# Kernel optimization log

Hardware: AMD Instinct MI355X
Metric: run time of the kernel (lower is better)

The kernel has to match this reference:

```python
import jax, jax.numpy as jnp
import numpy as np
from functools import partial

HEADS = 16
EPS = 1e-12  # torch F.normalize eps


def _l2_normalize(z):
    n = jnp.linalg.norm(z, axis=-1, keepdims=True)
    return z / jnp.maximum(n, EPS)


def setup_inputs() -> dict:
    key = jax.random.key(0)
    kx, kq, kk, kv, ko, kf = jax.random.split(key, 6)
    B, S, D, L = 2, 2048, 1024, 1024
    scale = 0.02
    return {
        "x": jax.random.normal(kx, (B, S, D), dtype=jnp.float32),
        "Wq": jax.random.normal(kq, (D, L), dtype=jnp.float32) * scale,
        "Wk": jax.random.normal(kk, (D, L), dtype=jnp.float32) * scale,
        "Wv": jax.random.normal(kv, (D, L), dtype=jnp.float32) * scale,
        "Wo": jax.random.normal(ko, (L, D), dtype=jnp.float32) * scale,
        "Wff": jax.random.normal(kf, (D, D), dtype=jnp.float32) * scale,
    }


def reference(x, Wq, Wk, Wv, Wo, Wff):
    B, S, D = x.shape
    H = HEADS
    L = Wq.shape[1]
    dh = L // H

    def split_heads(t):  # [B,S,L] -> [B*H, S, dh]  ('b y (h x) -> (b h) y x')
        return t.reshape(B, S, H, dh).transpose(0, 2, 1, 3).reshape(B * H, S, dh)

    q = split_heads(x @ Wq)
    k = split_heads(x @ Wk)
    v = split_heads(x @ Wv)

    # scores[b, k, q] = <q_q, k_k> / sqrt(input_size)  (note: scale uses D, not dh)
    scores = jnp.einsum('bqd,bkd->bkq', q, k) / jnp.sqrt(jnp.asarray(D, x.dtype))
    # faithful quirk: softmax over the LAST axis, which here is the query axis
    attn = jax.nn.softmax(scores, axis=-1)  # [B*H, K, Q]
    # out[b, q, d] = sum_k attn[b, k, q] * v[b, k, d]
    out = jnp.einsum('bkq,bkv->bqv', attn, v)  # [B*H, S, dh]

    # '(b h) y x -> b y (h x)'
    z = out.reshape(B, H, S, dh).transpose(0, 2, 1, 3).reshape(B, S, L)
    z = z @ Wo  # output projection (dropout is identity in eval)

    z = _l2_normalize(z)          # F.normalize after attention
    z = z @ Wff                   # FFNN linear (bias=False, dropout=identity)
    z = _l2_normalize(z)          # FFNN normalize (n_dim=-1)
    z = jax.nn.gelu(z, approximate=False)  # torch nn.GELU default = exact erf
    return z
```

## Files before the change

### kernel.cpp

```cpp
#include <hip/hip_runtime.h>
#include <hip/hip_bf16.h>
#include <stdint.h>


typedef __attribute__((ext_vector_type(8))) short short8;
typedef __attribute__((ext_vector_type(4))) float floatx4;

#define MFMA_BF16(a, b, c) __builtin_amdgcn_mfma_f32_16x16x32_bf16((a), (b), (c), 0, 0, 0)

__device__ __forceinline__ float bf2f(unsigned short u) {
  union { unsigned int i; float f; } v; v.i = ((unsigned int)u) << 16; return v.f;
}
__device__ __forceinline__ unsigned short f2bf(float f) {
  __hip_bfloat16 h = __float2bfloat16(f);
  return *reinterpret_cast<unsigned short*>(&h);
}
__device__ __forceinline__ void gld_lds16(const void* g, void* l) {
  __builtin_amdgcn_global_load_lds((__attribute__((address_space(1))) void*)g,
                                   (__attribute__((address_space(3))) void*)l,
                                   16, 0, 0);
}

__global__ __launch_bounds__(256) void detect_dtype(const unsigned int* __restrict__ x,
                                                    int* __restrict__ flag)
{
  __shared__ int red[4];
  int ok = 0;
  for (int i = 0; i < 16; ++i) {
    const unsigned int w = x[threadIdx.x * 16 + i];
    const unsigned int e = (w >> 7) & 0xFF;
    ok += (e == 0 || (e >= 96 && e <= 144)) ? 1 : 0;
  }
  for (int off = 32; off > 0; off >>= 1) ok += __shfl_down(ok, off, 64);
  if ((threadIdx.x & 63) == 0) red[threadIdx.x >> 6] = ok;
  __syncthreads();
  if (threadIdx.x == 0)
    *flag = ((red[0] + red[1] + red[2] + red[3]) > 2048) ? 1 : 0;
}

__global__ __launch_bounds__(256) void cvt_x(const void* __restrict__ src,
                                             unsigned short* __restrict__ dst,
                                             const int* __restrict__ flag)
{
  const int i = blockIdx.x * 256 + threadIdx.x;
  if (*flag) {
    ((uint4*)dst)[i] = ((const uint4*)src)[i];
  } else {
    const float4 a = ((const float4*)src)[2 * i];
    const float4 b = ((const float4*)src)[2 * i + 1];
    unsigned short o[8] = {f2bf(a.x), f2bf(a.y), f2bf(a.z), f2bf(a.w),
                           f2bf(b.x), f2bf(b.y), f2bf(b.z), f2bf(b.w)};
    ((uint4*)dst)[i] = *(uint4*)o;
  }
}

__global__ __launch_bounds__(256) void gemm_bt_128x64(
    const unsigned short* __restrict__ A, const unsigned short* __restrict__ Bt,
    unsigned short* __restrict__ C, int M, int N, int K, int lda, int ldb, int ldc)
{
  __shared__ __align__(16) unsigned short sA[128 * 32];
  __shared__ __align__(16) unsigned short sB[64 * 32];
  const int tid = threadIdx.x;
  const int wave = tid >> 6, lane = tid & 63, l15 = lane & 15, quad = lane >> 4;
  const int m0 = blockIdx.x * 128, n0 = blockIdx.y * 64;

  const floatx4 z4 = {0.f, 0.f, 0.f, 0.f};
  floatx4 acc[2][4];
  for (int i = 0; i < 2; ++i) for (int j = 0; j < 4; ++j) acc[i][j] = z4;

  const int NK = K >> 5;
  auto stage = [&](int kt) {
    const int k0 = kt << 5;
    for (int j = 0; j < 2; ++j) {
      const int ci = j * 256 + wave * 64 + lane;
      gld_lds16(A + (size_t)(m0 + (ci >> 2)) * lda + k0 + (ci & 3) * 8,
                &sA[(j * 256 + wave * 64) * 8]);
    }
    {
      const int ci = wave * 64 + lane;
      gld_lds16(Bt + (size_t)(n0 + (ci >> 2)) * ldb + k0 + (ci & 3) * 8,
                &sB[(wave * 64) * 8]);
    }
  };

  stage(0);
  for (int kt = 0; kt < NK; ++kt) {
    __syncthreads();
    short8 af[2], bf[4];
    for (int mt = 0; mt < 2; ++mt)
      af[mt] = *(const short8*)&sA[(wave * 32 + mt * 16 + l15) * 32 + quad * 8];
    for (int nt = 0; nt < 4; ++nt)
      bf[nt] = *(const short8*)&sB[(nt * 16 + l15) * 32 + quad * 8];
    for (int mt = 0; mt < 2; ++mt)
      for (int nt = 0; nt < 4; ++nt)
        acc[mt][nt] = MFMA_BF16(af[mt], bf[nt], acc[mt][nt]);
    __syncthreads();
    if (kt + 1 < NK) stage(kt + 1);
  }
  for (int mt = 0; mt < 2; ++mt)
    for (int nt = 0; nt < 4; ++nt)
      for (int r = 0; r < 4; ++r) {
        const int row = m0 + wave * 32 + mt * 16 + quad * 4 + r;
        const int col = n0 + nt * 16 + l15;
        C[(size_t)row * ldc + col] = f2bf(acc[mt][nt][r]);
      }
}

__global__ __launch_bounds__(256) void w_transpose(const void* __restrict__ W,
                                                   unsigned short* __restrict__ WT,
                                                   const int* __restrict__ flag)
{
  __shared__ __align__(16) unsigned short tile[64 * 72];
  const int rb = blockIdx.x * 64, cb = blockIdx.y * 64;
  const int tid = threadIdx.x;
  const int r = tid >> 2, c = tid & 3;
  unsigned short tmp[16];
  if (*flag) {
    const unsigned short* src = (const unsigned short*)W + (size_t)(rb + r) * 1024 + cb + c * 16;
    *(uint4*)&tmp[0] = *(const uint4*)src;
    *(uint4*)&tmp[8] = *(const uint4*)(src + 8);
  } else {
    const float* src = (const float*)W + (size_t)(rb + r) * 1024 + cb + c * 16;
    for (int j = 0; j < 16; j += 4) {
      const float4 f = *(const float4*)(src + j);
      tmp[j + 0] = f2bf(f.x); tmp[j + 1] = f2bf(f.y);
      tmp[j + 2] = f2bf(f.z); tmp[j + 3] = f2bf(f.w);
    }
  }
  *(uint4*)&tile[r * 72 + c * 16] = *(uint4*)&tmp[0];
  *(uint4*)&tile[r * 72 + c * 16 + 8] = *(uint4*)&tmp[8];
  __syncthreads();
  const int oc = tid >> 2;
  unsigned short out[16];
  for (int j = 0; j < 16; ++j) out[j] = tile[(c * 16 + j) * 72 + oc];
  unsigned short* dst = WT + (size_t)(cb + oc) * 1024 + rb + c * 16;
  *(uint4*)dst = *(uint4*)&out[0];
  *(uint4*)(dst + 8) = *(uint4*)&out[8];
}

__global__ __launch_bounds__(256) void v_transpose(const unsigned short* __restrict__ QKV,
                                                   unsigned short* __restrict__ Vt)
{
  __shared__ __align__(16) unsigned short tile[64 * 72];
  const int bh = blockIdx.x, st = blockIdx.y;
  const int b = bh >> 4, h = bh & 15;
  const int tid = threadIdx.x;
  const int r = tid >> 2, c = tid & 3;
  const unsigned short* src =
      QKV + (size_t)(b * 2048 + st * 64 + r) * 3072 + 2048 + h * 64 + c * 16;
  *(uint4*)&tile[r * 72 + c * 16] = *(const uint4*)src;
  *(uint4*)&tile[r * 72 + c * 16 + 8] = *(const uint4*)(src + 8);
  __syncthreads();
  const int d = tid >> 2;
  unsigned short out[16];
  for (int j = 0; j < 16; ++j) out[j] = tile[(c * 16 + j) * 72 + d];
  unsigned short* dst = Vt + (size_t)bh * 64 * 2048 + (size_t)d * 2048 + st * 64 + c * 16;
  *(uint4*)dst = *(uint4*)&out[0];
  *(uint4*)(dst + 8) = *(uint4*)&out[8];
}

__global__ __launch_bounds__(256) void attn_stats(const unsigned short* __restrict__ QKV,
                                                  float* __restrict__ spart)
{
  __shared__ __align__(16) unsigned short sQ[2][8 * 512];
  const int bh = blockIdx.x, kb = blockIdx.y, qs = blockIdx.z;
  const int b = bh >> 4, h = bh & 15;
  const int tid = threadIdx.x;
  const int wave = tid >> 6, lane = tid & 63, l15 = lane & 15, quad = lane >> 4;
  const int kbase = kb * 128 + wave * 32;
  const size_t row0 = (size_t)b * 2048;
  const int qoff = h * 64, koff = 1024 + h * 64;
  const int qbase = qs * 512;

  short8 kf[2][2];
  for (int rt = 0; rt < 2; ++rt)
    for (int ks = 0; ks < 2; ++ks)
      kf[rt][ks] = *(const short8*)&QKV[(row0 + kbase + rt * 16 + l15) * 3072 +
                                        koff + ks * 32 + quad * 8];

  float l[2][4];
  for (int rt = 0; rt < 2; ++rt)
    for (int r = 0; r < 4; ++r) l[rt][r] = 0.f;

  auto stageQ = [&](int t) {
    const int qt0 = qbase + t * 64;
    for (int j = 0; j < 2; ++j) {
      const int f = wave * 2 + j;
      const int nt = f >> 1, ks = f & 1;
      gld_lds16(QKV + (row0 + qt0 + nt * 16 + l15) * 3072 + qoff + ks * 32 + quad * 8,
                &sQ[t & 1][f * 512]);
    }
  };

  const floatx4 z4 = {0.f, 0.f, 0.f, 0.f};
  stageQ(0);
  for (int t = 0; t < 8; ++t) {
    __syncthreads();
    if (t + 1 < 8) stageQ(t + 1);
    const unsigned short* sQt = sQ[t & 1];
    for (int nt = 0; nt < 4; ++nt) {
      const short8 bq0 = *(const short8*)&sQt[(nt * 2 + 0) * 512 + lane * 8];
      const short8 bq1 = *(const short8*)&sQt[(nt * 2 + 1) * 512 + lane * 8];
      for (int rt = 0; rt < 2; ++rt) {
        floatx4 acc = z4;
        acc = MFMA_BF16(kf[rt][0], bq0, acc);
        acc = MFMA_BF16(kf[rt][1], bq1, acc);
        for (int r = 0; r < 4; ++r)
          l[rt][r] += __expf(acc[r] * 0.03125f);
      }
    }
  }
  for (int rt = 0; rt < 2; ++rt)
    for (int r = 0; r < 4; ++r) {
      float ll = l[rt][r];
      ll += __shfl_xor(ll, 1, 64);
      ll += __shfl_xor(ll, 2, 64);
      ll += __shfl_xor(ll, 4, 64);
      ll += __shfl_xor(ll, 8, 64);
      if (l15 == 0) {
        const int krow = kbase + rt * 16 + quad * 4 + r;
        spart[(size_t)qs * 65536 + bh * 2048 + krow] = ll;
      }
    }
}

__global__ __launch_bounds__(256) void stats_combine(const float* __restrict__ spart,
                                                     float* __restrict__ rsum)
{
  const int i = blockIdx.x * 256 + threadIdx.x;
  rsum[i] = 1.0f / (spart[i] + spart[i + 65536] + spart[i + 131072] + spart[i + 196608]);
}

__global__ __launch_bounds__(256) void attn_pv(const unsigned short* __restrict__ QKV,
                                               const unsigned short* __restrict__ Vt,
                                               const float* __restrict__ rsum,
                                               unsigned short* __restrict__ Z1)
{
  __shared__ __align__(16) unsigned short sK[64 * 64];
  __shared__ __align__(16) unsigned short sV[64 * 64];
  __shared__ __align__(16) unsigned short sP[64 * 72];
  const int bh = blockIdx.x, qb = blockIdx.y;
  const int b = bh >> 4, h = bh & 15;
  const int tid = threadIdx.x;
  const int wave = tid >> 6, lane = tid & 63, l15 = lane & 15, quad = lane >> 4;
  const size_t row0 = (size_t)b * 2048;
  const int qoff = h * 64, koff = 1024 + h * 64;
  const int q0 = qb * 64;
  const int srow = lane >> 3, schk = (lane & 7) ^ ((lane >> 3) & 7);

  short8 qf[2];
  for (int ks = 0; ks < 2; ++ks)
    qf[ks] = *(const short8*)&QKV[(row0 + q0 + wave * 16 + l15) * 3072 +
                                  qoff + ks * 32 + quad * 8];

  const floatx4 z4 = {0.f, 0.f, 0.f, 0.f};
  floatx4 acco[4];
  for (int j = 0; j < 4; ++j) acco[j] = z4;

  const unsigned short* VtB = Vt + (size_t)bh * 64 * 2048;
  const float* rsB = rsum + bh * 2048;

  for (int kt = 0; kt < 32; ++kt) {
    const int kb = kt * 64;
    __syncthreads();
    for (int j = 0; j < 2; ++j) {
      const int jj = wave * 2 + j;
      gld_lds16(QKV + (row0 + kb + jj * 8 + srow) * 3072 + koff + schk * 8, &sK[jj * 512]);
      gld_lds16(VtB + (size_t)(jj * 8 + srow) * 2048 + kb + schk * 8, &sV[jj * 512]);
    }
    __syncthreads();
    floatx4 sacc[4];
    for (int nt = 0; nt < 4; ++nt) {
      floatx4 a = z4;
      for (int ks = 0; ks < 2; ++ks) {
        const int row = nt * 16 + l15;
        const int chk = (ks * 4 + quad) ^ (l15 & 7);
        const short8 kfr = *(const short8*)&sK[row * 64 + chk * 8];
        a = MFMA_BF16(qf[ks], kfr, a);
      }
      sacc[nt] = a;
    }
    for (int nt = 0; nt < 4; ++nt) {
      const float rc = rsB[kb + nt * 16 + l15];
      for (int r = 0; r < 4; ++r) {
        const float p = __expf(sacc[nt][r] * 0.03125f) * rc;
        sP[(wave * 16 + quad * 4 + r) * 72 + nt * 16 + l15] = f2bf(p);
      }
    }
    __syncthreads();
    for (int ks = 0; ks < 2; ++ks) {
      const short8 pf = *(const short8*)&sP[(wave * 16 + l15) * 72 + ks * 32 + quad * 8];
      for (int nt = 0; nt < 4; ++nt) {
        const int row = nt * 16 + l15;
        const int chk = (ks * 4 + quad) ^ (l15 & 7);
        const short8 vf = *(const short8*)&sV[row * 64 + chk * 8];
        acco[nt] = MFMA_BF16(pf, vf, acco[nt]);
      }
    }
  }
  for (int nt = 0; nt < 4; ++nt)
    for (int r = 0; r < 4; ++r) {
      const int q = q0 + wave * 16 + quad * 4 + r;
      const int d = nt * 16 + l15;
      Z1[(row0 + q) * 1024 + qoff + d] = f2bf(acco[nt][r]);
    }
}

__global__ __launch_bounds__(256) void l2norm_gelu(const unsigned short* __restrict__ in,
                                                   void* __restrict__ out, int do_gelu,
                                                   int fin, const int* __restrict__ flag)
{
  __shared__ float red[4];
  const int row = blockIdx.x, tid = threadIdx.x;
  const unsigned short* p = in + (size_t)row * 1024 + tid * 4;
  const ushort4 u = *(const ushort4*)p;
  float x[4] = {bf2f(u.x), bf2f(u.y), bf2f(u.z), bf2f(u.w)};
  float ss = x[0] * x[0] + x[1] * x[1] + x[2] * x[2] + x[3] * x[3];
  for (int off = 32; off > 0; off >>= 1) ss += __shfl_down(ss, off, 64);
  if ((tid & 63) == 0) red[tid >> 6] = ss;
  __syncthreads();
  const float tot = red[0] + red[1] + red[2] + red[3];
  const float sc = 1.0f / fmaxf(sqrtf(tot), 1e-12f);
  float y[4];
  for (int j = 0; j < 4; ++j) {
    y[j] = x[j] * sc;
    if (do_gelu) y[j] = 0.5f * y[j] * (1.0f + erff(y[j] * 0.70710678118654752f));
  }
  if (fin && *flag == 0) {
    float4 o = {y[0], y[1], y[2], y[3]};
    ((float4*)out)[(size_t)row * 256 + tid] = o;
  } else {
    ushort4 o = {f2bf(y[0]), f2bf(y[1]), f2bf(y[2]), f2bf(y[3])};
    ((ushort4*)out)[(size_t)row * 256 + tid] = o;
  }
}

extern "C" void kernel_launch(void* const* d_in, const int* in_sizes, int n_in,
                              void* d_out, int out_size, void* d_ws, size_t ws_size,
                              hipStream_t stream)
{
  const void* x   = d_in[0];
  const void* Wq  = d_in[1];
  const void* Wk  = d_in[2];
  const void* Wv  = d_in[3];
  const void* Wo  = d_in[4];
  const void* Wff = d_in[5];

  char* ws = (char*)d_ws;
  size_t off = 0;
  auto alloc = [&](size_t bytes) -> void* {
    void* p = ws + off; off += (bytes + 255) & ~(size_t)255; return p;
  };
  int* flag             = (int*)alloc(256);
  unsigned short* xb    = (unsigned short*)alloc((size_t)4096 * 1024 * 2);
  unsigned short* WTqkv = (unsigned short*)alloc((size_t)3072 * 1024 * 2);
  unsigned short* WoT   = (unsigned short*)alloc((size_t)1024 * 1024 * 2);
  unsigned short* WffT  = (unsigned short*)alloc((size_t)1024 * 1024 * 2);
  unsigned short* QKV   = (unsigned short*)alloc((size_t)4096 * 3072 * 2);
  unsigned short* Vt    = (unsigned short*)alloc((size_t)32 * 64 * 2048 * 2);
  float* spart          = (float*)alloc((size_t)4 * 65536 * 4);
  float* rsum           = (float*)alloc((size_t)65536 * 4);
  unsigned short* z1    = (unsigned short*)alloc((size_t)4096 * 1024 * 2);
  unsigned short* z2  = Vt;
  unsigned short* z2n = xb;
  unsigned short* z3  = QKV;

  detect_dtype<<<1, 256, 0, stream>>>((const unsigned int*)x, flag);
  cvt_x<<<2048, 256, 0, stream>>>(x, xb, flag);

  w_transpose<<<dim3(16, 16), 256, 0, stream>>>(Wq, WTqkv, flag);
  w_transpose<<<dim3(16, 16), 256, 0, stream>>>(Wk, WTqkv + (size_t)1024 * 1024, flag);
  w_transpose<<<dim3(16, 16), 256, 0, stream>>>(Wv, WTqkv + (size_t)2048 * 1024, flag);
  w_transpose<<<dim3(16, 16), 256, 0, stream>>>(Wo, WoT, flag);
  w_transpose<<<dim3(16, 16), 256, 0, stream>>>(Wff, WffT, flag);

  gemm_bt_128x64<<<dim3(32, 48), 256, 0, stream>>>(xb, WTqkv, QKV,
                                                   4096, 3072, 1024, 1024, 1024, 3072);
  v_transpose<<<dim3(32, 32), 256, 0, stream>>>(QKV, Vt);
  attn_stats<<<dim3(32, 16, 4), 256, 0, stream>>>(QKV, spart);
  stats_combine<<<256, 256, 0, stream>>>(spart, rsum);
  attn_pv<<<dim3(32, 32), 256, 0, stream>>>(QKV, Vt, rsum, z1);

  gemm_bt_128x64<<<dim3(32, 16), 256, 0, stream>>>(z1, WoT, z2,
                                                   4096, 1024, 1024, 1024, 1024, 1024);
  l2norm_gelu<<<4096, 256, 0, stream>>>(z2, z2n, 0, 0, flag);
  gemm_bt_128x64<<<dim3(32, 16), 256, 0, stream>>>(z2n, WffT, z3,
                                                   4096, 1024, 1024, 1024, 1024, 1024);
  l2norm_gelu<<<4096, 256, 0, stream>>>(z3, d_out, 1, 1, flag);
}
```

Baseline: 322.3 us.

## Fold softmax scale into Q, pre-normalize V, double-buffer attn_pv, merge weight transposes

The QKV GEMM epilogue now multiplies the Q columns by 1/32·log2(e), so both attention kernels can use a raw exp2 instead of a scaled expf. The per-key softmax reciprocal is applied to V during its transpose, which is moved after the stats kernels, and this removes the rsum load and multiply from the attn_pv inner loop. attn_pv double-buffers its K/V tiles, cuts the __syncthreads calls per tile, and processes the P tile in two 32-key halves with a smaller LDS buffer. The five weight-transpose launches are merged into one 3D-grid launch. Rounding Q after scaling and rounding the scaled V to bf16 changes numerics slightly.

```diff
diff --git a/kernel.cpp b/kernel.cpp
--- a/kernel.cpp
+++ b/kernel.cpp
@@ -7,6 +7,15 @@
 typedef __attribute__((ext_vector_type(4))) float floatx4;
 
 #define MFMA_BF16(a, b, c) __builtin_amdgcn_mfma_f32_16x16x32_bf16((a), (b), (c), 0, 0, 0)
+
+#if defined(__has_builtin)
+#if __has_builtin(__builtin_amdgcn_exp2f)
+#define EXP2F(x) __builtin_amdgcn_exp2f(x)
+#endif
+#endif
+#ifndef EXP2F
+#define EXP2F(x) __expf((x) * 0.69314718056f)
+#endif
 
 __device__ __forceinline__ float bf2f(unsigned short u) {
   union { unsigned int i; float f; } v; v.i = ((unsigned int)u) << 16; return v.f;
@@ -56,7 +65,8 @@
 
 __global__ __launch_bounds__(256) void gemm_bt_128x64(
     const unsigned short* __restrict__ A, const unsigned short* __restrict__ Bt,
-    unsigned short* __restrict__ C, int M, int N, int K, int lda, int ldb, int ldc)
+    unsigned short* __restrict__ C, int M, int N, int K, int lda, int ldb, int ldc,
+    int qscale_cols)
 {
   __shared__ __align__(16) unsigned short sA[128 * 32];
   __shared__ __align__(16) unsigned short sB[64 * 32];
@@ -102,15 +112,22 @@
       for (int r = 0; r < 4; ++r) {
         const int row = m0 + wave * 32 + mt * 16 + quad * 4 + r;
         const int col = n0 + nt * 16 + l15;
-        C[(size_t)row * ldc + col] = f2bf(acc[mt][nt][r]);
+        float v = acc[mt][nt][r];
+        if (col < qscale_cols) v *= 0.04508422f;
+        C[(size_t)row * ldc + col] = f2bf(v);
       }
 }
 
-__global__ __launch_bounds__(256) void w_transpose(const void* __restrict__ W,
-                                                   unsigned short* __restrict__ WT,
-                                                   const int* __restrict__ flag)
+__global__ __launch_bounds__(256) void w_transpose5(
+    const void* __restrict__ W0, const void* __restrict__ W1,
+    const void* __restrict__ W2, const void* __restrict__ W3,
+    const void* __restrict__ W4, unsigned short* __restrict__ WT,
+    const int* __restrict__ flag)
 {
   __shared__ __align__(16) unsigned short tile[64 * 72];
+  const void* srcs[5] = {W0, W1, W2, W3, W4};
+  const void* W = srcs[blockIdx.z];
+  unsigned short* dst0 = WT + (size_t)blockIdx.z * 1024 * 1024;
   const int rb = blockIdx.x * 64, cb = blockIdx.y * 64;
   const int tid = threadIdx.x;
   const int r = tid >> 2, c = tid & 3;
@@ -133,12 +150,13 @@
   const int oc = tid >> 2;
   unsigned short out[16];
   for (int j = 0; j < 16; ++j) out[j] = tile[(c * 16 + j) * 72 + oc];
-  unsigned short* dst = WT + (size_t)(cb + oc) * 1024 + rb + c * 16;
+  unsigned short* dst = dst0 + (size_t)(cb + oc) * 1024 + rb + c * 16;
   *(uint4*)dst = *(uint4*)&out[0];
   *(uint4*)(dst + 8) = *(uint4*)&out[8];
 }
 
 __global__ __launch_bounds__(256) void v_transpose(const unsigned short* __restrict__ QKV,
+                                                   const float* __restrict__ rsum,
                                                    unsigned short* __restrict__ Vt)
 {
   __shared__ __align__(16) unsigned short tile[64 * 72];
@@ -152,8 +170,10 @@
   *(uint4*)&tile[r * 72 + c * 16 + 8] = *(const uint4*)(src + 8);
   __syncthreads();
   const int d = tid >> 2;
+  const float* rsB = rsum + bh * 2048 + st * 64 + c * 16;
   unsigned short out[16];
-  for (int j = 0; j < 16; ++j) out[j] = tile[(c * 16 + j) * 72 + d];
+  for (int j = 0; j < 16; ++j)
+    out[j] = f2bf(bf2f(tile[(c * 16 + j) * 72 + d]) * rsB[j]);
   unsigned short* dst = Vt + (size_t)bh * 64 * 2048 + (size_t)d * 2048 + st * 64 + c * 16;
   *(uint4*)dst = *(uint4*)&out[0];
   *(uint4*)(dst + 8) = *(uint4*)&out[8];
@@ -206,7 +226,7 @@
         acc = MFMA_BF16(kf[rt][0], bq0, acc);
         acc = MFMA_BF16(kf[rt][1], bq1, acc);
         for (int r = 0; r < 4; ++r)
-          l[rt][r] += __expf(acc[r] * 0.03125f);
+          l[rt][r] += EXP2F(acc[r]);
       }
     }
   }
@@ -233,12 +253,11 @@
 
 __global__ __launch_bounds__(256) void attn_pv(const unsigned short* __restrict__ QKV,
                                                const unsigned short* __restrict__ Vt,
-                                               const float* __restrict__ rsum,
                                                unsigned short* __restrict__ Z1)
 {
-  __shared__ __align__(16) unsigned short sK[64 * 64];
-  __shared__ __align__(16) unsigned short sV[64 * 64];
-  __shared__ __align__(16) unsigned short sP[64 * 72];
+  __shared__ __align__(16) unsigned short sK[2][64 * 64];
+  __shared__ __align__(16) unsigned short sV[2][64 * 64];
+  __shared__ __align__(16) unsigned short sP[64 * 36];
   const int bh = blockIdx.x, qb = blockIdx.y;
   const int b = bh >> 4, h = bh & 15;
   const int tid = threadIdx.x;
@@ -258,43 +277,44 @@
   for (int j = 0; j < 4; ++j) acco[j] = z4;
 
   const unsigned short* VtB = Vt + (size_t)bh * 64 * 2048;
-  const float* rsB = rsum + bh * 2048;
-
-  for (int kt = 0; kt < 32; ++kt) {
+
+  auto stage = [&](int kt) {
     const int kb = kt * 64;
-    __syncthreads();
+    const int bufi = kt & 1;
     for (int j = 0; j < 2; ++j) {
       const int jj = wave * 2 + j;
-      gld_lds16(QKV + (row0 + kb + jj * 8 + srow) * 3072 + koff + schk * 8, &sK[jj * 512]);
-      gld_lds16(VtB + (size_t)(jj * 8 + srow) * 2048 + kb + schk * 8, &sV[jj * 512]);
-    }
+      gld_lds16(QKV + (row0 + kb + jj * 8 + srow) * 3072 + koff + schk * 8,
+                &sK[bufi][jj * 512]);
+      gld_lds16(VtB + (size_t)(jj * 8 + srow) * 2048 + kb + schk * 8,
+                &sV[bufi][jj * 512]);
+    }
+  };
+
+  stage(0);
+  for (int kt = 0; kt < 32; ++kt) {
     __syncthreads();
-    floatx4 sacc[4];
-    for (int nt = 0; nt < 4; ++nt) {
-      floatx4 a = z4;
-      for (int ks = 0; ks < 2; ++ks) {
-        const int row = nt * 16 + l15;
-        const int chk = (ks * 4 + quad) ^ (l15 & 7);
-        const short8 kfr = *(const short8*)&sK[row * 64 + chk * 8];
-        a = MFMA_BF16(qf[ks], kfr, a);
+    if (kt + 1 < 32) stage(kt + 1);
+    const unsigned short* sKt = sK[kt & 1];
+    const unsigned short* sVt = sV[kt & 1];
+    for (int h2 = 0; h2 < 2; ++h2) {
+      floatx4 sacc[2];
+      for (int nt2 = 0; nt2 < 2; ++nt2) {
+        floatx4 a = z4;
+        for (int ks = 0; ks < 2; ++ks) {
+          const int row = h2 * 32 + nt2 * 16 + l15;
+          const int chk = (ks * 4 + quad) ^ (l15 & 7);
+          a = MFMA_BF16(qf[ks], *(const short8*)&sKt[row * 64 + chk * 8], a);
+        }
+        sacc[nt2] = a;
       }
-      sacc[nt] = a;
-    }
-    for (int nt = 0; nt < 4; ++nt) {
-      const float rc = rsB[kb + nt * 16 + l15];
-      for (int r = 0; r < 4; ++r) {
-        const float p = __expf(sacc[nt][r] * 0.03125f) * rc;
-        sP[(wave * 16 + quad * 4 + r) * 72 + nt * 16 + l15] = f2bf(p);
-      }
-    }
-    __syncthreads();
-    for (int ks = 0; ks < 2; ++ks) {
-      const short8 pf = *(const short8*)&sP[(wave * 16 + l15) * 72 + ks * 32 + quad * 8];
+      for (int nt2 = 0; nt2 < 2; ++nt2)
+        for (int r = 0; r < 4; ++r)
+          sP[(wave * 16 + quad * 4 + r) * 36 + nt2 * 16 + l15] = f2bf(EXP2F(sacc[nt2][r]));
+      const short8 pf = *(const short8*)&sP[(wave * 16 + l15) * 36 + quad * 8];
       for (int nt = 0; nt < 4; ++nt) {
         const int row = nt * 16 + l15;
-        const int chk = (ks * 4 + quad) ^ (l15 & 7);
-        const short8 vf = *(const short8*)&sV[row * 64 + chk * 8];
-        acco[nt] = MFMA_BF16(pf, vf, acco[nt]);
+        const int chk = (h2 * 4 + quad) ^ (l15 & 7);
+        acco[nt] = MFMA_BF16(pf, *(const short8*)&sVt[row * 64 + chk * 8], acco[nt]);
       }
     }
   }
@@ -353,38 +373,34 @@
   };
   int* flag             = (int*)alloc(256);
   unsigned short* xb    = (unsigned short*)alloc((size_t)4096 * 1024 * 2);
-  unsigned short* WTqkv = (unsigned short*)alloc((size_t)3072 * 1024 * 2);
-  unsigned short* WoT   = (unsigned short*)alloc((size_t)1024 * 1024 * 2);
-  unsigned short* WffT  = (unsigned short*)alloc((size_t)1024 * 1024 * 2);
+  unsigned short* WT    = (unsigned short*)alloc((size_t)5 * 1024 * 1024 * 2);
   unsigned short* QKV   = (unsigned short*)alloc((size_t)4096 * 3072 * 2);
   unsigned short* Vt    = (unsigned short*)alloc((size_t)32 * 64 * 2048 * 2);
   float* spart          = (float*)alloc((size_t)4 * 65536 * 4);
   float* rsum           = (float*)alloc((size_t)65536 * 4);
   unsigned short* z1    = (unsigned short*)alloc((size_t)4096 * 1024 * 2);
+  unsigned short* WTqkv = WT;
+  unsigned short* WoT   = WT + (size_t)3 * 1024 * 1024;
+  unsigned short* WffT  = WT + (size_t)4 * 1024 * 1024;
   unsigned short* z2  = Vt;
   unsigned short* z2n = xb;
   unsigned short* z3  = QKV;
 
   detect_dtype<<<1, 256, 0, stream>>>((const unsigned int*)x, flag);
   cvt_x<<<2048, 256, 0, stream>>>(x, xb, flag);
-
-  w_transpose<<<dim3(16, 16), 256, 0, stream>>>(Wq, WTqkv, flag);
-  w_transpose<<<dim3(16, 16), 256, 0, stream>>>(Wk, WTqkv + (size_t)1024 * 1024, flag);
-  w_transpose<<<dim3(16, 16), 256, 0, stream>>>(Wv, WTqkv + (size_t)2048 * 1024, flag);
-  w_transpose<<<dim3(16, 16), 256, 0, stream>>>(Wo, WoT, flag);
-  w_transpose<<<dim3(16, 16), 256, 0, stream>>>(Wff, WffT, flag);
+  w_transpose5<<<dim3(16, 16, 5), 256, 0, stream>>>(Wq, Wk, Wv, Wo, Wff, WT, flag);
 
   gemm_bt_128x64<<<dim3(32, 48), 256, 0, stream>>>(xb, WTqkv, QKV,
-                                                   4096, 3072, 1024, 1024, 1024, 3072);
-  v_transpose<<<dim3(32, 32), 256, 0, stream>>>(QKV, Vt);
+                                                   4096, 3072, 1024, 1024, 1024, 3072, 1024);
   attn_stats<<<dim3(32, 16, 4), 256, 0, stream>>>(QKV, spart);
   stats_combine<<<256, 256, 0, stream>>>(spart, rsum);
-  attn_pv<<<dim3(32, 32), 256, 0, stream>>>(QKV, Vt, rsum, z1);
+  v_transpose<<<dim3(32, 32), 256, 0, stream>>>(QKV, rsum, Vt);
+  attn_pv<<<dim3(32, 32), 256, 0, stream>>>(QKV, Vt, z1);
 
   gemm_bt_128x64<<<dim3(32, 16), 256, 0, stream>>>(z1, WoT, z2,
-                                                   4096, 1024, 1024, 1024, 1024, 1024);
+                                                   4096, 1024, 1024, 1024, 1024, 1024, 0);
   l2norm_gelu<<<4096, 256, 0, stream>>>(z2, z2n, 0, 0, flag);
   gemm_bt_128x64<<<dim3(32, 16), 256, 0, stream>>>(z2n, WffT, z3,
-                                                   4096, 1024, 1024, 1024, 1024, 1024);
+                                                   4096, 1024, 1024, 1024, 1024, 1024, 0);
   l2norm_gelu<<<4096, 256, 0, stream>>>(z3, d_out, 1, 1, flag);
 }
```

Result: faster. 300.8 us (-6.7%).
